# Kernel tuning notes

Measured on AMD Instinct MI355X. Metric: run time of the kernel, lower is better.

The kernel has to match this reference:

```python
import jax, jax.numpy as jnp
import numpy as np

D_STATE = 4
DT_RANK = 4  # ceil(64/16)
D_INNER = 64


def conv1d(x, w, b, pad):
    # x: [B,C,L], w: [O,I,K]
    y = jax.lax.conv_general_dilated(x, w, (1,), [(pad, pad)],
                                     dimension_numbers=('NCH', 'OIH', 'NCH'))
    return y + b[None, :, None]


def maxpool2(x):
    B, C, L = x.shape
    return x.reshape(B, C, L // 2, 2).max(-1)


def layernorm(x, g, b):
    m = x.mean(-1, keepdims=True)
    v = ((x - m) ** 2).mean(-1, keepdims=True)
    return (x - m) / jnp.sqrt(v + 1e-5) * g + b


def mamba_block(x, in_w, cv_w, cv_b, xp_w, dt_w, dt_b, A_log, Dp, out_w):
    # x: [B,L,d_model]; d_inner == d_model (expand=1)
    B, L, _ = x.shape
    xz = jnp.einsum('bld,ed->ble', x, in_w)          # [B,L,2*d_inner]
    xi, z = jnp.split(xz, 2, axis=-1)
    # causal depthwise conv, kernel size 2
    xc = jax.lax.conv_general_dilated(xi.transpose(0, 2, 1), cv_w, (1,), [(1, 0)],
                                      feature_group_count=D_INNER,
                                      dimension_numbers=('NCH', 'OIH', 'NCH'))
    u = jax.nn.silu(xc + cv_b[None, :, None]).transpose(0, 2, 1)  # [B,L,d_inner]
    x_dbl = jnp.einsum('bld,ed->ble', u, xp_w)        # [B,L,dt_rank+2*d_state]
    dt, Bm, Cm = jnp.split(x_dbl, [DT_RANK, DT_RANK + D_STATE], axis=-1)
    dt = jax.nn.softplus(jnp.einsum('blr,dr->bld', dt, dt_w) + dt_b)  # [B,L,d_inner]
    A = -jnp.exp(A_log)                               # [d_inner, d_state]
    dA = jnp.exp(dt[..., None] * A)                   # [B,L,d_inner,d_state]
    dBu = dt[..., None] * Bm[:, :, None, :] * u[..., None]

    def step(h, inp):
        dA_t, dBu_t, C_t = inp
        h = dA_t * h + dBu_t                          # [B,d_inner,d_state]
        y = jnp.einsum('bdn,bn->bd', h, C_t)
        return h, y

    h0 = jnp.zeros((B, D_INNER, D_STATE), x.dtype)
    _, ys = jax.lax.scan(step, h0, (dA.transpose(1, 0, 2, 3),
                                    dBu.transpose(1, 0, 2, 3),
                                    Cm.transpose(1, 0, 2)))
    y = ys.transpose(1, 0, 2) + Dp * u                # skip connection D*u
    y = y * jax.nn.silu(z)
    return jnp.einsum('bld,ed->ble', y, out_w)


def setup_inputs() -> dict:
    key = jax.random.key(0)
    ks = jax.random.split(key, 32)
    n = lambda k, s, sc=0.05: (jax.random.normal(k, s, jnp.float32) * sc)
    inp = {
        'x': jax.random.normal(ks[0], (512, 1, 4096), jnp.float32),
        'c1w': n(ks[1], (16, 1, 5), 0.3), 'c1b': n(ks[2], (16,)),
        'c2w': n(ks[3], (32, 16, 5), 0.1), 'c2b': n(ks[4], (32,)),
        'c3w': n(ks[5], (64, 32, 5), 0.08), 'c3b': n(ks[6], (64,)),
        'lw': n(ks[7], (4096, 2048), 0.02), 'lb': n(ks[8], (4096,)),
    }
    A_init = jnp.log(jnp.tile(jnp.arange(1, D_STATE + 1, dtype=jnp.float32), (D_INNER, 1)))
    for i, base in ((1, 9), (2, 20)):
        inp[f'ln{i}g'] = jnp.ones((64,), jnp.float32)
        inp[f'ln{i}b'] = jnp.zeros((64,), jnp.float32)
        inp[f'in{i}w'] = n(ks[base + 0], (2 * D_INNER, 64), 0.08)
        inp[f'cv{i}w'] = n(ks[base + 1], (D_INNER, 1, 2), 0.3)
        inp[f'cv{i}b'] = n(ks[base + 2], (D_INNER,))
        inp[f'xp{i}w'] = n(ks[base + 3], (DT_RANK + 2 * D_STATE, D_INNER), 0.08)
        inp[f'dt{i}w'] = n(ks[base + 4], (D_INNER, DT_RANK), 0.3)
        inp[f'dt{i}b'] = n(ks[base + 5], (D_INNER,), 0.5)
        inp[f'al{i}'] = A_init
        inp[f'dp{i}'] = jnp.ones((D_INNER,), jnp.float32)
        inp[f'ow{i}'] = n(ks[base + 6], (64, D_INNER), 0.08)
    return inp


def reference(x, c1w, c1b, c2w, c2b, c3w, c3b, lw, lb,
              ln1g, ln1b, in1w, cv1w, cv1b, xp1w, dt1w, dt1b, al1, dp1, ow1,
              ln2g, ln2b, in2w, cv2w, cv2b, xp2w, dt2w, dt2b, al2, dp2, ow2):
    B = x.shape[0]
    h = maxpool2(jax.nn.relu(conv1d(x, c1w, c1b, 2)))       # [B,16,L/2]
    h = maxpool2(jax.nn.relu(conv1d(h, c2w, c2b, 2)))       # [B,32,L/4]
    h = jax.nn.relu(conv1d(h, c3w, c3b, 2))                 # [B,64,L/4]
    # AdaptiveAvgPool1d(32): L/4 divisible by 32 -> exact window means
    L4 = h.shape[-1]
    h = h.reshape(B, 64, 32, L4 // 32).mean(-1)             # [B,64,32]
    h = h.reshape(B, -1)                                    # [B,2048]
    h = (h @ lw.T + lb).reshape(B, 64, 64)                  # [B,64,64]
    h = mamba_block(layernorm(h, ln1g, ln1b), in1w, cv1w, cv1b, xp1w, dt1w, dt1b, al1, dp1, ow1)
    h = mamba_block(layernorm(h, ln2g, ln2b), in2w, cv2w, cv2b, xp2w, dt2w, dt2b, al2, dp2, ow2)
    return h
```

## Files before the change

### kernel.cpp

```cpp
#include <hip/hip_runtime.h>
#include <hip/hip_bf16.h>
#include <math.h>

#define NB 512

typedef __attribute__((ext_vector_type(8))) short short8;
typedef __attribute__((ext_vector_type(4))) float f32x4;
union U4 { uint4 u; short8 s8; };
union BF { __hip_bfloat16 h; ushort us; };

__device__ __forceinline__ int swz(int u) { return u ^ ((u >> 3) & 7); }
__device__ __forceinline__ int idx8(int l, int u) { return l * 8 + (u ^ (l & 7)); }

__global__ __launch_bounds__(256) void prep_all(const float4* __restrict__ lw4,
                                                ushort4* __restrict__ lwb4,
                                                const float* __restrict__ w2,
                                                __hip_bfloat16* __restrict__ w2b,
                                                const float* __restrict__ w3,
                                                __hip_bfloat16* __restrict__ w3b,
                                                const float* __restrict__ in1w,
                                                const float* __restrict__ in2w,
                                                __hip_bfloat16* __restrict__ winb,
                                                const float* __restrict__ ow1,
                                                const float* __restrict__ ow2,
                                                __hip_bfloat16* __restrict__ owb) {
    int blk = blockIdx.x, t = threadIdx.x;
    if (blk < 8192) {
        int i = blk * 256 + t;
        float4 v = lw4[i];
        union { ushort4 u; __hip_bfloat16 h[4]; } o;
        o.h[0] = __float2bfloat16(v.x);
        o.h[1] = __float2bfloat16(v.y);
        o.h[2] = __float2bfloat16(v.z);
        o.h[3] = __float2bfloat16(v.w);
        lwb4[i] = o.u;
    } else if (blk == 8192) {
        for (int i = t; i < 3072; i += 256) {
            int c2 = i / 96, rest = i - c2 * 96;
            int tp = rest >> 5, r2 = rest & 31;
            int tl = r2 >> 4, c1 = r2 & 15;
            int tap = tp * 2 + tl;
            float v = (tap < 5) ? w2[c2 * 80 + c1 * 5 + tap] : 0.f;
            w2b[i] = __float2bfloat16(v);
        }
        for (int i = t; i < 10240; i += 256) {
            int c3 = i / 160, rest = i - c3 * 160;
            int kk = rest >> 5, c1 = rest & 31;
            w3b[i] = __float2bfloat16(w3[c3 * 160 + c1 * 5 + kk]);
        }
    } else {
        for (int i = t; i < 16384; i += 256)
            winb[i] = __float2bfloat16((i < 8192 ? in1w : in2w)[i & 8191]);
        for (int i = t; i < 8192; i += 256)
            owb[i] = __float2bfloat16((i < 4096 ? ow1 : ow2)[i & 4095]);
    }
}

__global__ __launch_bounds__(256) void conv_trunk(const float* __restrict__ x,
                                                  const float* __restrict__ c1w,
                                                  const float* __restrict__ c1b,
                                                  const __hip_bfloat16* __restrict__ w2b,
                                                  const float* __restrict__ c2b,
                                                  const __hip_bfloat16* __restrict__ w3b,
                                                  const float* __restrict__ c3b,
                                                  __hip_bfloat16* __restrict__ h3b) {
    __shared__ uint4 H1u[2200];
    __shared__ uint4 H2u[2176];
    float* xs = (float*)H2u;
    int t = threadIdx.x, h = blockIdx.x, b = blockIdx.y;
    int lane = t & 63, w = t >> 6, m = lane & 15, quad = lane >> 4;
    int p0 = 1024 * h - 6;

    const float* xb = x + b * 4096;
    int gbase = 2 * p0 - 2;
    for (int i = t; i < 2200; i += 256) {
        int gx = gbase + i;
        xs[i] = (gx >= 0 && gx < 4096) ? xb[gx] : 0.f;
    }
    U4 Bf2[3][2];
    {
        const uint4* wsrc = (const uint4*)w2b;
#pragma unroll
        for (int ct = 0; ct < 2; ++ct)
#pragma unroll
            for (int tp = 0; tp < 3; ++tp)
                Bf2[tp][ct].u = wsrc[(ct * 16 + m) * 12 + tp * 4 + quad];
    }
    float bv2[2];
#pragma unroll
    for (int ct = 0; ct < 2; ++ct) bv2[ct] = c2b[ct * 16 + m];
    float wv[80], bv1[16];
#pragma unroll
    for (int i = 0; i < 80; ++i) wv[i] = c1w[i];
#pragma unroll
    for (int i = 0; i < 16; ++i) bv1[i] = c1b[i];
    __syncthreads();

    for (int r = t; r < 1096; r += 256) {
        int p = p0 + r;
        union { uint4 q[2]; __hip_bfloat16 hh[16]; } o;
        if (p >= 0 && p < 2048) {
            const float* s = xs + 2 * r;
            float s0 = s[0], s1 = s[1], s2 = s[2], s3 = s[3], s4 = s[4], s5 = s[5];
#pragma unroll
            for (int c = 0; c < 16; ++c) {
                const float* wr = wv + c * 5;
                float v0 = fmaf(wr[0], s0, fmaf(wr[1], s1, fmaf(wr[2], s2, fmaf(wr[3], s3, fmaf(wr[4], s4, bv1[c])))));
                float v1 = fmaf(wr[0], s1, fmaf(wr[1], s2, fmaf(wr[2], s3, fmaf(wr[3], s4, fmaf(wr[4], s5, bv1[c])))));
                o.hh[c] = __float2bfloat16(fmaxf(fmaxf(v0, v1), 0.f));
            }
        } else {
            o.q[0] = (uint4){0, 0, 0, 0};
            o.q[1] = (uint4){0, 0, 0, 0};
        }
        H1u[swz(2 * r)] = o.q[0];
        H1u[swz(2 * r + 1)] = o.q[1];
    }
    __syncthreads();

    __hip_bfloat16* H2h = (__hip_bfloat16*)H2u;
    for (int g = w; g < 68; g += 4) {
        f32x4 acc[2];
#pragma unroll
        for (int ct = 0; ct < 2; ++ct) acc[ct] = (f32x4){bv2[ct], bv2[ct], bv2[ct], bv2[ct]};
#pragma unroll
        for (int tp = 0; tp < 3; ++tp) {
            int u = 2 * (g * 16 + m + 2 * tp) + quad;
            U4 av; av.u = H1u[swz(u)];
            acc[0] = __builtin_amdgcn_mfma_f32_16x16x32_bf16(av.s8, Bf2[tp][0].s8, acc[0], 0, 0, 0);
            acc[1] = __builtin_amdgcn_mfma_f32_16x16x32_bf16(av.s8, Bf2[tp][1].s8, acc[1], 0, 0, 0);
        }
        int pp = g * 8 + quad * 2;
#pragma unroll
        for (int ct = 0; ct < 2; ++ct) {
            float o0 = fmaxf(fmaxf(acc[ct][0], acc[ct][1]), 0.f);
            float o1 = fmaxf(fmaxf(acc[ct][2], acc[ct][3]), 0.f);
            int ch = ct * 16 + m;
            int u0 = pp * 4 + (ch >> 3);
            H2h[swz(u0) * 8 + (ch & 7)] = __float2bfloat16(o0);
            H2h[swz(u0 + 4) * 8 + (ch & 7)] = __float2bfloat16(o1);
        }
    }
    __syncthreads();
    if (t < 8) {
        int row = (h == 0) ? (t >> 2) : (514 + (t >> 2));
        H2u[swz(row * 4 + (t & 3))] = (uint4){0, 0, 0, 0};
    }
    __syncthreads();

    U4 Bf3[5][4];
    {
        const uint4* wsrc = (const uint4*)w3b;
#pragma unroll
        for (int ct = 0; ct < 4; ++ct)
#pragma unroll
            for (int kk = 0; kk < 5; ++kk)
                Bf3[kk][ct].u = wsrc[(ct * 16 + m) * 20 + kk * 4 + quad];
    }
    float bv3[4];
#pragma unroll
    for (int ct = 0; ct < 4; ++ct) bv3[ct] = c3b[ct * 16 + m];

    for (int ii = 0; ii < 4; ++ii) {
        int wl = w * 4 + ii;
        float sum[4] = {0.f, 0.f, 0.f, 0.f};
#pragma unroll
        for (int half = 0; half < 2; ++half) {
            int gp = wl * 2 + half;
            f32x4 acc[4];
#pragma unroll
            for (int ct = 0; ct < 4; ++ct) acc[ct] = (f32x4){bv3[ct], bv3[ct], bv3[ct], bv3[ct]};
#pragma unroll
            for (int kk = 0; kk < 5; ++kk) {
                int u = 4 * (gp * 16 + m + kk) + quad;
                U4 av; av.u = H2u[swz(u)];
#pragma unroll
                for (int ct = 0; ct < 4; ++ct)
                    acc[ct] = __builtin_amdgcn_mfma_f32_16x16x32_bf16(av.s8, Bf3[kk][ct].s8, acc[ct], 0, 0, 0);
            }
#pragma unroll
            for (int ct = 0; ct < 4; ++ct) {
                sum[ct] += fmaxf(acc[ct][0], 0.f) + fmaxf(acc[ct][1], 0.f)
                         + fmaxf(acc[ct][2], 0.f) + fmaxf(acc[ct][3], 0.f);
            }
        }
#pragma unroll
        for (int ct = 0; ct < 4; ++ct) {
            float s = sum[ct];
            s += __shfl_xor(s, 16, 64);
            s += __shfl_xor(s, 32, 64);
            sum[ct] = s;
        }
        float sv = (quad == 0) ? sum[0] : (quad == 1) ? sum[1] : (quad == 2) ? sum[2] : sum[3];
        int win = h * 16 + wl;
        h3b[b * 2048 + (quad * 16 + m) * 32 + win] = __float2bfloat16(sv * (1.f / 32.f));
    }
}

__global__ __launch_bounds__(256) void lin_gemm_mfma(const __hip_bfloat16* __restrict__ A,
                                                     const __hip_bfloat16* __restrict__ B,
                                                     const float* __restrict__ bias,
                                                     float* __restrict__ C) {
    __shared__ uint4 A_s[512];
    __shared__ uint4 B_s[512];
    int t = threadIdx.x;
    int col0 = blockIdx.x * 64;
    int row0 = blockIdx.y * 64;
    int w = t >> 6, lane = t & 63;
    int m = lane & 15, quad = lane >> 4;
    int lh = w >> 1, eh = w & 1;

    f32x4 acc[2][2];
#pragma unroll
    for (int li = 0; li < 2; ++li)
#pragma unroll
        for (int ei = 0; ei < 2; ++ei) acc[li][ei] = (f32x4){0.f, 0.f, 0.f, 0.f};

    for (int ki = 0; ki < 32; ++ki) {
        int k0 = ki * 64;
#pragma unroll
        for (int p = 0; p < 2; ++p) {
            int id = p * 256 + t;
            int r = id >> 3, u = id & 7;
            A_s[r * 8 + (u ^ (r & 7))] = *(const uint4*)(A + (row0 + r) * 2048 + k0 + u * 8);
            B_s[r * 8 + (u ^ (r & 7))] = *(const uint4*)(B + (size_t)(col0 + r) * 2048 + k0 + u * 8);
        }
        __syncthreads();
#pragma unroll
        for (int c = 0; c < 2; ++c) {
            int uu = c * 4 + quad;
            U4 av[2], bv[2];
#pragma unroll
            for (int li = 0; li < 2; ++li) {
                int ra = (lh * 2 + li) * 16 + m;
                av[li].u = A_s[ra * 8 + (uu ^ (ra & 7))];
            }
#pragma unroll
            for (int ei = 0; ei < 2; ++ei) {
                int rb = (eh * 2 + ei) * 16 + m;
                bv[ei].u = B_s[rb * 8 + (uu ^ (rb & 7))];
            }
#pragma unroll
            for (int li = 0; li < 2; ++li)
#pragma unroll
                for (int ei = 0; ei < 2; ++ei)
                    acc[li][ei] = __builtin_amdgcn_mfma_f32_16x16x32_bf16(av[li].s8, bv[ei].s8, acc[li][ei], 0, 0, 0);
        }
        __syncthreads();
    }
#pragma unroll
    for (int li = 0; li < 2; ++li)
#pragma unroll
        for (int ei = 0; ei < 2; ++ei) {
            int col = col0 + (eh * 2 + ei) * 16 + m;
            float bvv = bias[col];
#pragma unroll
            for (int reg = 0; reg < 4; ++reg) {
                int row = row0 + (lh * 2 + li) * 16 + quad * 4 + reg;
                C[row * 4096 + col] = acc[li][ei][reg] + bvv;
            }
        }
}

struct MambaP {
    const float *lng, *lnb, *cvw, *cvb, *xpw, *dtw, *dtb, *al, *dp;
};

__global__ __launch_bounds__(256) void mamba2_kernel(const float* __restrict__ lin,
                                                     const __hip_bfloat16* __restrict__ winb,
                                                     const __hip_bfloat16* __restrict__ owb,
                                                     MambaP p1, MambaP p2,
                                                     float* __restrict__ out) {
    __shared__ float X[64][68];
    __shared__ float XI[64][68];
    __shared__ float DTS[64][68];
    __shared__ float W12[64][14];
    __shared__ uint4 XBu[512];
    int b = blockIdx.x, t = threadIdx.x;
    int lane = t & 63, w = t >> 6, m = lane & 15, quad = lane >> 4;
    int l0 = w * 16;

    {
        const float4* lin4 = (const float4*)(lin + b * 4096);
        for (int i = t; i < 1024; i += 256) {
            float4 v = lin4[i];
            *(float4*)(&X[i >> 4][(i & 15) * 4]) = v;
        }
    }
    __syncthreads();

    for (int blk = 0; blk < 2; ++blk) {
        MambaP P = blk ? p2 : p1;

        {
            int l = t >> 2, q = t & 3;
            float4 xv[4];
            const float4* xr = (const float4*)(&X[l][q * 16]);
#pragma unroll
            for (int j = 0; j < 4; ++j) xv[j] = xr[j];
            float s = 0.f;
#pragma unroll
            for (int j = 0; j < 4; ++j) s += (xv[j].x + xv[j].y) + (xv[j].z + xv[j].w);
            s += __shfl_xor(s, 1, 4);
            s += __shfl_xor(s, 2, 4);
            float mm = s * (1.f / 64.f);
            float v = 0.f;
#pragma unroll
            for (int j = 0; j < 4; ++j) {
                float dx;
                dx = xv[j].x - mm; v = fmaf(dx, dx, v);
                dx = xv[j].y - mm; v = fmaf(dx, dx, v);
                dx = xv[j].z - mm; v = fmaf(dx, dx, v);
                dx = xv[j].w - mm; v = fmaf(dx, dx, v);
            }
            v += __shfl_xor(v, 1, 4);
            v += __shfl_xor(v, 2, 4);
            float rstd = rsqrtf(v * (1.f / 64.f) + 1e-5f);
            const float4* g4 = (const float4*)(P.lng + q * 16);
            const float4* bb4 = (const float4*)(P.lnb + q * 16);
            union { uint4 qq[2]; __hip_bfloat16 hh[16]; } o;
#pragma unroll
            for (int j = 0; j < 4; ++j) {
                float4 g = g4[j], bb = bb4[j];
                o.hh[j * 4 + 0] = __float2bfloat16((xv[j].x - mm) * rstd * g.x + bb.x);
                o.hh[j * 4 + 1] = __float2bfloat16((xv[j].y - mm) * rstd * g.y + bb.y);
                o.hh[j * 4 + 2] = __float2bfloat16((xv[j].z - mm) * rstd * g.z + bb.z);
                o.hh[j * 4 + 3] = __float2bfloat16((xv[j].w - mm) * rstd * g.w + bb.w);
            }
            XBu[idx8(l, q * 2)] = o.qq[0];
            XBu[idx8(l, q * 2 + 1)] = o.qq[1];
        }
        __syncthreads();

        {
            const uint4* wp = (const uint4*)winb + blk * 1024;
            U4 Bf[8][2];
#pragma unroll
            for (int nt = 0; nt < 8; ++nt)
#pragma unroll
                for (int c = 0; c < 2; ++c)
                    Bf[nt][c].u = wp[(nt * 16 + m) * 8 + c * 4 + quad];
            f32x4 acc[8];
#pragma unroll
            for (int nt = 0; nt < 8; ++nt) acc[nt] = (f32x4){0.f, 0.f, 0.f, 0.f};
#pragma unroll
            for (int c = 0; c < 2; ++c) {
                U4 av; av.u = XBu[idx8(l0 + m, c * 4 + quad)];
#pragma unroll
                for (int nt = 0; nt < 8; ++nt)
                    acc[nt] = __builtin_amdgcn_mfma_f32_16x16x32_bf16(av.s8, Bf[nt][c].s8, acc[nt], 0, 0, 0);
            }
#pragma unroll
            for (int nt = 0; nt < 4; ++nt)
#pragma unroll
                for (int reg = 0; reg < 4; ++reg)
                    XI[l0 + quad * 4 + reg][nt * 16 + m] = acc[nt][reg];
#pragma unroll
            for (int nt = 4; nt < 8; ++nt)
#pragma unroll
                for (int reg = 0; reg < 4; ++reg)
                    X[l0 + quad * 4 + reg][(nt - 4) * 16 + m] = acc[nt][reg];
        }
        __syncthreads();

        {
            int d = t & 63, lg = t >> 6;
            int lc = lg * 16;
            float cur[16];
            float prev = (lc == 0) ? 0.f : XI[lc - 1][d];
#pragma unroll
            for (int j = 0; j < 16; ++j) cur[j] = XI[lc + j][d];
            __syncthreads();
            float w0 = P.cvw[d * 2], w1 = P.cvw[d * 2 + 1], cb = P.cvb[d];
#pragma unroll
            for (int j = 0; j < 16; ++j) {
                float xp = (j == 0) ? prev : cur[j - 1];
                float v = fmaf(w0, xp, fmaf(w1, cur[j], cb));
                XI[lc + j][d] = v / (1.f + __expf(-v));
            }
        }
        __syncthreads();

        {
            int l = t & 63, jg = t >> 6;
            float4 xrow[16];
            const float4* xr = (const float4*)(&XI[l][0]);
#pragma unroll
            for (int k4 = 0; k4 < 16; ++k4) xrow[k4] = xr[k4];
#pragma unroll
            for (int jj = 0; jj < 3; ++jj) {
                int j = jg * 3 + jj;
                const float4* wr = (const float4*)(P.xpw + j * 64);
                float a0 = 0.f, a1 = 0.f, a2 = 0.f, a3 = 0.f;
#pragma unroll
                for (int k4 = 0; k4 < 16; ++k4) {
                    float4 wvv = wr[k4];
                    a0 = fmaf(xrow[k4].x, wvv.x, a0);
                    a1 = fmaf(xrow[k4].y, wvv.y, a1);
                    a2 = fmaf(xrow[k4].z, wvv.z, a2);
                    a3 = fmaf(xrow[k4].w, wvv.w, a3);
                }
                float accv = (a0 + a1) + (a2 + a3);
                int slot = (j < 4) ? j : ((j < 8) ? (4 + (j - 4) * 2) : (5 + (j - 8) * 2));
                W12[l][slot] = accv;
            }
        }
        __syncthreads();

        {
            int l = t & 63, dg = t >> 6;
            float d0 = W12[l][0], d1 = W12[l][1], d2 = W12[l][2], d3 = W12[l][3];
#pragma unroll 4
            for (int jj = 0; jj < 16; ++jj) {
                int d = dg * 16 + jj;
                const float4 wvv = *(const float4*)(P.dtw + d * 4);
                float xdt = fmaf(wvv.x, d0, fmaf(wvv.y, d1, fmaf(wvv.z, d2, fmaf(wvv.w, d3, P.dtb[d]))));
                DTS[d][l] = fmaxf(xdt, 0.f) + __logf(1.f + __expf(-fabsf(xdt)));
            }
        }
        __syncthreads();

        {
            int d = t >> 2, n = t & 3;
            float Aval = -__expf(P.al[d * 4 + n]);
            float dpv = P.dp[d];
            const float* dtrow = &DTS[d][0];
            ushort* YBh = (ushort*)XBu;
            int ybase = 0;
            float h = 0.f;
            for (int l = 0; l < 64; ++l) {
                float dtv = dtrow[l];
                float dA = __expf(dtv * Aval);
                float uv = XI[l][d];
                float2 bc = *(const float2*)(&W12[l][4 + n * 2]);
                h = fmaf(dA, h, dtv * bc.x * uv);
                float part = h * bc.y;
                part += __shfl_xor(part, 1, 4);
                part += __shfl_xor(part, 2, 4);
                if (n == 0) {
                    float zv = X[l][d];
                    float yv = part + dpv * uv;
                    float gy = yv * (zv / (1.f + __expf(-zv)));
                    BF cv; cv.h = __float2bfloat16(gy);
                    YBh[idx8(l, d >> 3) * 8 + (d & 7)] = cv.us;
                }
                (void)ybase;
            }
        }
        __syncthreads();

        {
            const uint4* wp = (const uint4*)owb + blk * 512;
            U4 Bf[4][2];
#pragma unroll
            for (int nt = 0; nt < 4; ++nt)
#pragma unroll
                for (int c = 0; c < 2; ++c)
                    Bf[nt][c].u = wp[(nt * 16 + m) * 8 + c * 4 + quad];
            f32x4 acc[4];
#pragma unroll
            for (int nt = 0; nt < 4; ++nt) acc[nt] = (f32x4){0.f, 0.f, 0.f, 0.f};
#pragma unroll
            for (int c = 0; c < 2; ++c) {
                U4 av; av.u = XBu[idx8(l0 + m, c * 4 + quad)];
#pragma unroll
                for (int nt = 0; nt < 4; ++nt)
                    acc[nt] = __builtin_amdgcn_mfma_f32_16x16x32_bf16(av.s8, Bf[nt][c].s8, acc[nt], 0, 0, 0);
            }
            if (blk == 0) {
#pragma unroll
                for (int nt = 0; nt < 4; ++nt)
#pragma unroll
                    for (int reg = 0; reg < 4; ++reg)
                        X[l0 + quad * 4 + reg][nt * 16 + m] = acc[nt][reg];
            } else {
                float* ob = out + b * 4096;
#pragma unroll
                for (int nt = 0; nt < 4; ++nt)
#pragma unroll
                    for (int reg = 0; reg < 4; ++reg)
                        ob[(l0 + quad * 4 + reg) * 64 + nt * 16 + m] = acc[nt][reg];
            }
        }
        __syncthreads();
    }
}

extern "C" void kernel_launch(void* const* d_in, const int* in_sizes, int n_in,
                              void* d_out, int out_size, void* d_ws, size_t ws_size,
                              hipStream_t stream) {
    const float* x   = (const float*)d_in[0];
    const float* c1w = (const float*)d_in[1];
    const float* c1b = (const float*)d_in[2];
    const float* c2w = (const float*)d_in[3];
    const float* c2b = (const float*)d_in[4];
    const float* c3w = (const float*)d_in[5];
    const float* c3b = (const float*)d_in[6];
    const float* lw  = (const float*)d_in[7];
    const float* lb  = (const float*)d_in[8];

    MambaP p1, p2;
    p1.lng = (const float*)d_in[9];  p1.lnb = (const float*)d_in[10];
    p1.cvw = (const float*)d_in[12]; p1.cvb = (const float*)d_in[13];
    p1.xpw = (const float*)d_in[14]; p1.dtw = (const float*)d_in[15];
    p1.dtb = (const float*)d_in[16]; p1.al  = (const float*)d_in[17];
    p1.dp  = (const float*)d_in[18];
    p2.lng = (const float*)d_in[20]; p2.lnb = (const float*)d_in[21];
    p2.cvw = (const float*)d_in[23]; p2.cvb = (const float*)d_in[24];
    p2.xpw = (const float*)d_in[25]; p2.dtw = (const float*)d_in[26];
    p2.dtb = (const float*)d_in[27]; p2.al  = (const float*)d_in[28];
    p2.dp  = (const float*)d_in[29];
    const float* in1w = (const float*)d_in[11];
    const float* in2w = (const float*)d_in[22];
    const float* ow1  = (const float*)d_in[19];
    const float* ow2  = (const float*)d_in[30];

    const size_t MB = 1024 * 1024;
    char* base = (char*)d_ws;
    __hip_bfloat16* lwb  = (__hip_bfloat16*)base;
    __hip_bfloat16* h3b  = (__hip_bfloat16*)(base + 16 * MB);
    float* lin           = (float*)(base + 20 * MB);
    __hip_bfloat16* w2b  = (__hip_bfloat16*)(base + 28 * MB);
    __hip_bfloat16* w3b  = (__hip_bfloat16*)(base + 28 * MB + 64 * 1024);
    __hip_bfloat16* winb = (__hip_bfloat16*)(base + 28 * MB + 256 * 1024);
    __hip_bfloat16* owb  = (__hip_bfloat16*)(base + 28 * MB + 512 * 1024);
    float* outp = (float*)d_out;

    prep_all<<<dim3(8194), dim3(256), 0, stream>>>((const float4*)lw, (ushort4*)lwb,
                                                   c2w, w2b, c3w, w3b,
                                                   in1w, in2w, winb, ow1, ow2, owb);
    conv_trunk<<<dim3(2, NB), dim3(256), 0, stream>>>(x, c1w, c1b, w2b, c2b, w3b, c3b, h3b);
    lin_gemm_mfma<<<dim3(64, 8), dim3(256), 0, stream>>>(h3b, lwb, lb, lin);
    mamba2_kernel<<<dim3(NB), dim3(256), 0, stream>>>(lin, winb, owb, p1, p2, outp);
}
```

Before: 287.2 us.

## Fuse linear-weight bf16 conversion into GEMM and split conv trunk finer

Drops the separate pass that converted the 4096x2048 linear weight to bf16 and instead converts fp32 weights on the fly inside the GEMM's tile loads. This saves a full write and reread of the bf16 weight copy, but each GEMM block now reads fp32 weights, which doubles that load traffic and adds conversion work. The conv trunk is split into four sequence chunks per batch instead of two, using smaller shared memory for more blocks and occupancy at the cost of more halo recompute. The scan loop also gets a partial unroll.

```diff
diff --git a/kernel.cpp b/kernel.cpp
--- a/kernel.cpp
+++ b/kernel.cpp
@@ -12,47 +12,35 @@
 __device__ __forceinline__ int swz(int u) { return u ^ ((u >> 3) & 7); }
 __device__ __forceinline__ int idx8(int l, int u) { return l * 8 + (u ^ (l & 7)); }
 
-__global__ __launch_bounds__(256) void prep_all(const float4* __restrict__ lw4,
-                                                ushort4* __restrict__ lwb4,
-                                                const float* __restrict__ w2,
-                                                __hip_bfloat16* __restrict__ w2b,
-                                                const float* __restrict__ w3,
-                                                __hip_bfloat16* __restrict__ w3b,
-                                                const float* __restrict__ in1w,
-                                                const float* __restrict__ in2w,
-                                                __hip_bfloat16* __restrict__ winb,
-                                                const float* __restrict__ ow1,
-                                                const float* __restrict__ ow2,
-                                                __hip_bfloat16* __restrict__ owb) {
-    int blk = blockIdx.x, t = threadIdx.x;
-    if (blk < 8192) {
-        int i = blk * 256 + t;
-        float4 v = lw4[i];
-        union { ushort4 u; __hip_bfloat16 h[4]; } o;
-        o.h[0] = __float2bfloat16(v.x);
-        o.h[1] = __float2bfloat16(v.y);
-        o.h[2] = __float2bfloat16(v.z);
-        o.h[3] = __float2bfloat16(v.w);
-        lwb4[i] = o.u;
-    } else if (blk == 8192) {
-        for (int i = t; i < 3072; i += 256) {
-            int c2 = i / 96, rest = i - c2 * 96;
-            int tp = rest >> 5, r2 = rest & 31;
-            int tl = r2 >> 4, c1 = r2 & 15;
-            int tap = tp * 2 + tl;
-            float v = (tap < 5) ? w2[c2 * 80 + c1 * 5 + tap] : 0.f;
-            w2b[i] = __float2bfloat16(v);
-        }
-        for (int i = t; i < 10240; i += 256) {
-            int c3 = i / 160, rest = i - c3 * 160;
-            int kk = rest >> 5, c1 = rest & 31;
-            w3b[i] = __float2bfloat16(w3[c3 * 160 + c1 * 5 + kk]);
-        }
+__global__ __launch_bounds__(256) void prep_w(const float* __restrict__ w2,
+                                              __hip_bfloat16* __restrict__ w2b,
+                                              const float* __restrict__ w3,
+                                              __hip_bfloat16* __restrict__ w3b,
+                                              const float* __restrict__ in1w,
+                                              const float* __restrict__ in2w,
+                                              __hip_bfloat16* __restrict__ winb,
+                                              const float* __restrict__ ow1,
+                                              const float* __restrict__ ow2,
+                                              __hip_bfloat16* __restrict__ owb) {
+    int i = blockIdx.x * 256 + threadIdx.x;
+    if (i < 3072) {
+        int c2 = i / 96, rest = i - c2 * 96;
+        int tp = rest >> 5, r2 = rest & 31;
+        int tl = r2 >> 4, c1 = r2 & 15;
+        int tap = tp * 2 + tl;
+        float v = (tap < 5) ? w2[c2 * 80 + c1 * 5 + tap] : 0.f;
+        w2b[i] = __float2bfloat16(v);
+    } else if (i < 13312) {
+        int j = i - 3072;
+        int c3 = j / 160, rest = j - c3 * 160;
+        int kk = rest >> 5, c1 = rest & 31;
+        w3b[j] = __float2bfloat16(w3[c3 * 160 + c1 * 5 + kk]);
+    } else if (i < 29696) {
+        int j = i - 13312;
+        winb[j] = __float2bfloat16((j < 8192 ? in1w : in2w)[j & 8191]);
     } else {
-        for (int i = t; i < 16384; i += 256)
-            winb[i] = __float2bfloat16((i < 8192 ? in1w : in2w)[i & 8191]);
-        for (int i = t; i < 8192; i += 256)
-            owb[i] = __float2bfloat16((i < 4096 ? ow1 : ow2)[i & 4095]);
+        int j = i - 29696;
+        owb[j] = __float2bfloat16((j < 4096 ? ow1 : ow2)[j & 4095]);
     }
 }
 
@@ -64,16 +52,16 @@
                                                   const __hip_bfloat16* __restrict__ w3b,
                                                   const float* __restrict__ c3b,
                                                   __hip_bfloat16* __restrict__ h3b) {
-    __shared__ uint4 H1u[2200];
-    __shared__ uint4 H2u[2176];
+    __shared__ uint4 H1u[1088];
+    __shared__ uint4 H2u[1088];
     float* xs = (float*)H2u;
     int t = threadIdx.x, h = blockIdx.x, b = blockIdx.y;
     int lane = t & 63, w = t >> 6, m = lane & 15, quad = lane >> 4;
-    int p0 = 1024 * h - 6;
+    int p0 = h * 512 - 6;
+    int gbase = h * 1024 - 14;
 
     const float* xb = x + b * 4096;
-    int gbase = 2 * p0 - 2;
-    for (int i = t; i < 2200; i += 256) {
+    for (int i = t; i < 1080; i += 256) {
         int gx = gbase + i;
         xs[i] = (gx >= 0 && gx < 4096) ? xb[gx] : 0.f;
     }
@@ -96,7 +84,7 @@
     for (int i = 0; i < 16; ++i) bv1[i] = c1b[i];
     __syncthreads();
 
-    for (int r = t; r < 1096; r += 256) {
+    for (int r = t; r < 536; r += 256) {
         int p = p0 + r;
         union { uint4 q[2]; __hip_bfloat16 hh[16]; } o;
         if (p >= 0 && p < 2048) {
@@ -119,7 +107,7 @@
     __syncthreads();
 
     __hip_bfloat16* H2h = (__hip_bfloat16*)H2u;
-    for (int g = w; g < 68; g += 4) {
+    for (int g = w; g < 33; g += 4) {
         f32x4 acc[2];
 #pragma unroll
         for (int ct = 0; ct < 2; ++ct) acc[ct] = (f32x4){bv2[ct], bv2[ct], bv2[ct], bv2[ct]};
@@ -142,10 +130,8 @@
         }
     }
     __syncthreads();
-    if (t < 8) {
-        int row = (h == 0) ? (t >> 2) : (514 + (t >> 2));
-        H2u[swz(row * 4 + (t & 3))] = (uint4){0, 0, 0, 0};
-    }
+    if (h == 0 && t < 8) H2u[swz((t >> 2) * 4 + (t & 3))] = (uint4){0, 0, 0, 0};
+    if (h == 3 && t < 8) H2u[swz((258 + (t >> 2)) * 4 + (t & 3))] = (uint4){0, 0, 0, 0};
     __syncthreads();
 
     U4 Bf3[5][4];
@@ -161,8 +147,9 @@
 #pragma unroll
     for (int ct = 0; ct < 4; ++ct) bv3[ct] = c3b[ct * 16 + m];
 
-    for (int ii = 0; ii < 4; ++ii) {
-        int wl = w * 4 + ii;
+#pragma unroll
+    for (int ww = 0; ww < 2; ++ww) {
+        int wl = w * 2 + ww;
         float sum[4] = {0.f, 0.f, 0.f, 0.f};
 #pragma unroll
         for (int half = 0; half < 2; ++half) {
@@ -192,13 +179,13 @@
             sum[ct] = s;
         }
         float sv = (quad == 0) ? sum[0] : (quad == 1) ? sum[1] : (quad == 2) ? sum[2] : sum[3];
-        int win = h * 16 + wl;
+        int win = h * 8 + wl;
         h3b[b * 2048 + (quad * 16 + m) * 32 + win] = __float2bfloat16(sv * (1.f / 32.f));
     }
 }
 
 __global__ __launch_bounds__(256) void lin_gemm_mfma(const __hip_bfloat16* __restrict__ A,
-                                                     const __hip_bfloat16* __restrict__ B,
+                                                     const float* __restrict__ Bw,
                                                      const float* __restrict__ bias,
                                                      float* __restrict__ C) {
     __shared__ uint4 A_s[512];
@@ -223,7 +210,14 @@
             int id = p * 256 + t;
             int r = id >> 3, u = id & 7;
             A_s[r * 8 + (u ^ (r & 7))] = *(const uint4*)(A + (row0 + r) * 2048 + k0 + u * 8);
-            B_s[r * 8 + (u ^ (r & 7))] = *(const uint4*)(B + (size_t)(col0 + r) * 2048 + k0 + u * 8);
+            const float4* s4 = (const float4*)(Bw + (size_t)(col0 + r) * 2048 + k0 + u * 8);
+            float4 f0 = s4[0], f1 = s4[1];
+            union { uint4 q; __hip_bfloat16 hh[8]; } o;
+            o.hh[0] = __float2bfloat16(f0.x); o.hh[1] = __float2bfloat16(f0.y);
+            o.hh[2] = __float2bfloat16(f0.z); o.hh[3] = __float2bfloat16(f0.w);
+            o.hh[4] = __float2bfloat16(f1.x); o.hh[5] = __float2bfloat16(f1.y);
+            o.hh[6] = __float2bfloat16(f1.z); o.hh[7] = __float2bfloat16(f1.w);
+            B_s[r * 8 + (u ^ (r & 7))] = o.q;
         }
         __syncthreads();
 #pragma unroll
@@ -426,8 +420,8 @@
             float dpv = P.dp[d];
             const float* dtrow = &DTS[d][0];
             ushort* YBh = (ushort*)XBu;
-            int ybase = 0;
             float h = 0.f;
+#pragma unroll 4
             for (int l = 0; l < 64; ++l) {
                 float dtv = dtrow[l];
                 float dA = __expf(dtv * Aval);
@@ -444,7 +438,6 @@
                     BF cv; cv.h = __float2bfloat16(gy);
                     YBh[idx8(l, d >> 3) * 8 + (d & 7)] = cv.us;
                 }
-                (void)ybase;
             }
         }
         __syncthreads();
@@ -517,19 +510,17 @@
 
     const size_t MB = 1024 * 1024;
     char* base = (char*)d_ws;
-    __hip_bfloat16* lwb  = (__hip_bfloat16*)base;
-    __hip_bfloat16* h3b  = (__hip_bfloat16*)(base + 16 * MB);
-    float* lin           = (float*)(base + 20 * MB);
-    __hip_bfloat16* w2b  = (__hip_bfloat16*)(base + 28 * MB);
-    __hip_bfloat16* w3b  = (__hip_bfloat16*)(base + 28 * MB + 64 * 1024);
-    __hip_bfloat16* winb = (__hip_bfloat16*)(base + 28 * MB + 256 * 1024);
-    __hip_bfloat16* owb  = (__hip_bfloat16*)(base + 28 * MB + 512 * 1024);
+    __hip_bfloat16* h3b  = (__hip_bfloat16*)base;
+    float* lin           = (float*)(base + 4 * MB);
+    __hip_bfloat16* w2b  = (__hip_bfloat16*)(base + 16 * MB);
+    __hip_bfloat16* w3b  = (__hip_bfloat16*)(base + 16 * MB + 64 * 1024);
+    __hip_bfloat16* winb = (__hip_bfloat16*)(base + 16 * MB + 256 * 1024);
+    __hip_bfloat16* owb  = (__hip_bfloat16*)(base + 16 * MB + 512 * 1024);
     float* outp = (float*)d_out;
 
-    prep_all<<<dim3(8194), dim3(256), 0, stream>>>((const float4*)lw, (ushort4*)lwb,
-                                                   c2w, w2b, c3w, w3b,
-                                                   in1w, in2w, winb, ow1, ow2, owb);
-    conv_trunk<<<dim3(2, NB), dim3(256), 0, stream>>>(x, c1w, c1b, w2b, c2b, w3b, c3b, h3b);
-    lin_gemm_mfma<<<dim3(64, 8), dim3(256), 0, stream>>>(h3b, lwb, lb, lin);
+    prep_w<<<dim3(148), dim3(256), 0, stream>>>(c2w, w2b, c3w, w3b,
+                                                in1w, in2w, winb, ow1, ow2, owb);
+    conv_trunk<<<dim3(4, NB), dim3(256), 0, stream>>>(x, c1w, c1b, w2b, c2b, w3b, c3b, h3b);
+    lin_gemm_mfma<<<dim3(64, 8), dim3(256), 0, stream>>>(h3b, lw, lb, lin);
     mamba2_kernel<<<dim3(NB), dim3(256), 0, stream>>>(lin, winb, owb, p1, p2, outp);
 }
```

Result: faster. 267.0 us (-7.0%).
